# Performance work log

Measured on AMD Instinct MI355X. Metric: run time of the kernel, lower is better.

Reference implementation:

```python
import jax, jax.numpy as jnp
import numpy as np

N, E, D, K, NCONV = 50000, 800000, 64, 3, 6


def setup_inputs() -> dict:
    key = jax.random.key(0)
    ks = jax.random.split(key, 6)
    X = jax.random.normal(ks[0], (N, D), jnp.float32)
    edge_index = jax.random.randint(ks[1], (2, E), 0, N, dtype=jnp.int64)
    edge_weight = jax.random.uniform(ks[2], (E,), jnp.float32)
    H = jax.random.normal(ks[3], (N, D), jnp.float32)
    lambda_max = jnp.ones((1,), jnp.float32) * 2.0  # typical sym-normalized Laplacian bound
    conv_w = jax.random.normal(ks[4], (NCONV, K, D, D), jnp.float32) / np.sqrt(D)
    conv_b = jnp.zeros((NCONV, D), jnp.float32)
    return {"X": X, "edge_index": edge_index, "edge_weight": edge_weight,
            "H": H, "lambda_max": lambda_max, "conv_w": conv_w, "conv_b": conv_b}


def reference(X, edge_index, edge_weight, H, lambda_max, conv_w, conv_b):
    src, dst = edge_index[0], edge_index[1]
    # symmetric normalization: norm_e = w_e / sqrt(deg_src * deg_dst)
    deg = jax.ops.segment_sum(edge_weight, src, num_segments=N)
    dinv = jnp.where(deg > 0, deg ** -0.5, 0.0)
    norm = edge_weight * dinv[src] * dinv[dst]  # [E]
    lam = lambda_max.reshape(())
    c = 2.0 / lam

    def a_prop(v):  # A_norm @ v via scatter-add over edges, [N,D]
        return jax.ops.segment_sum(norm[:, None] * v[src], dst, num_segments=N)

    def l_hat(v):  # (2/lam)(I - A_norm) v - v
        return (c - 1.0) * v - c * a_prop(v)

    def cheb(v, w, b):  # ChebConv order K: sum_k T_k(L_hat) v @ W_k + b
        tx0, tx1 = v, l_hat(v)
        out = tx0 @ w[0] + tx1 @ w[1]
        for k in range(2, K):
            tx2 = 2.0 * l_hat(tx1) - tx0
            out = out + tx2 @ w[k]
            tx0, tx1 = tx1, tx2
        return out + b

    Z = jax.nn.sigmoid(cheb(X, conv_w[0], conv_b[0]) + cheb(H, conv_w[1], conv_b[1]))
    R = jax.nn.sigmoid(cheb(X, conv_w[2], conv_b[2]) + cheb(H, conv_w[3], conv_b[3]))
    H_tilde = jnp.tanh(cheb(X, conv_w[4], conv_b[4]) + cheb(H * R, conv_w[5], conv_b[5]))
    return Z * H_tilde + (1.0 - Z) * H
```

## Files before the change

kernel.cpp:

```cpp
#include <hip/hip_runtime.h>
#include <cstdint>
#include <cstddef>

typedef unsigned int u32;
typedef unsigned short u16;
typedef unsigned long long u64;

#define D 64
#define NCH 512
#define CAP 5120

typedef __attribute__((ext_vector_type(8))) short bf16x8;
typedef __attribute__((ext_vector_type(4))) float f32x4;

static __device__ __forceinline__ float sigmoidf_(float x) {
    return 1.f / (1.f + __expf(-x));
}
static __device__ __forceinline__ u16 f2bf(float x) {
    u32 u = __float_as_uint(x);
    return (u16)((u + 0x7fffu + ((u >> 16) & 1u)) >> 16);
}
static __device__ __forceinline__ u32 packbf2(float a, float b) {
    return (u32)f2bf(a) | ((u32)f2bf(b) << 16);
}
static __device__ __forceinline__ float bflo(u32 u) { return __uint_as_float(u << 16); }
static __device__ __forceinline__ float bfhi(u32 u) { return __uint_as_float(u & 0xffff0000u); }


__global__ void init_kernel(u32* cur_d, u32* cur_s) {
    int t = threadIdx.x;
    cur_d[t] = (u32)(t * CAP);
    cur_s[t] = (u32)(t * CAP);
}

__global__ __launch_bounds__(256) void coarse_kernel(
    const int* __restrict__ src, const int* __restrict__ dst, const float* __restrict__ w,
    u32* cur_d, u32* cur_s,
    u64* __restrict__ slab_d, u32* __restrict__ slab_s,
    int E, int CE) {
    __shared__ u32 hd[256], hs[256], cd[256], cs[256];
    int t = threadIdx.x, c = blockIdx.x;
    hd[t] = 0; hs[t] = 0;
    __syncthreads();
    int e0 = c * CE, e1 = min(E, e0 + CE);
    for (int e = e0 + t; e < e1; e += 256) {
        atomicAdd(&hd[(u32)dst[e] >> 8], 1u);
        atomicAdd(&hs[(u32)src[e] >> 8], 1u);
    }
    __syncthreads();
    cd[t] = atomicAdd(&cur_d[t], hd[t]);
    cs[t] = atomicAdd(&cur_s[t], hs[t]);
    __syncthreads();
    for (int e = e0 + t; e < e1; e += 256) {
        int s = src[e], d = dst[e];
        u32 wb = (u32)f2bf(w[e]);
        u32 pd = atomicAdd(&cd[(u32)d >> 8], 1u);
        u32 ps = atomicAdd(&cs[(u32)s >> 8], 1u);
        if (pd < (u32)(((d >> 8) + 1) * CAP))
            slab_d[pd] = (u64)((u32)s | (((u32)d & 255u) << 16)) | ((u64)wb << 32);
        if (ps < (u32)(((s >> 8) + 1) * CAP))
            slab_s[ps] = ((u32)s & 255u) | (wb << 16);
    }
}

__global__ void bprefix_kernel(const u32* __restrict__ cur_d, u32* __restrict__ bstart, int NB) {
    __shared__ int sd[256];
    int t = threadIdx.x;
    int v = (t < NB) ? min((int)cur_d[t] - t * CAP, CAP) : 0;
    sd[t] = v;
    __syncthreads();
    for (int o = 1; o < 256; o <<= 1) {
        int a = (t >= o) ? sd[t - o] : 0;
        __syncthreads();
        sd[t] += a;
        __syncthreads();
    }
    bstart[t] = (u32)(sd[t] - v);
}

__global__ __launch_bounds__(256) void fine_dst_kernel(
    const u64* __restrict__ slab, const u32* __restrict__ cur_d,
    const u32* __restrict__ bstart, u32* __restrict__ edge4,
    int* __restrict__ cnt, int* __restrict__ row_start, int N_) {
    __shared__ int h[256], sd[256], cur[256];
    int b = blockIdx.x, t = threadIdx.x;
    int m = min((int)cur_d[b] - b * CAP, CAP);
    const u64* rp = slab + (size_t)b * CAP;
    h[t] = 0;
    __syncthreads();
    for (int i = t; i < m; i += 256) atomicAdd(&h[(int)((rp[i] >> 16) & 255u)], 1);
    __syncthreads();
    int v = h[t];
    sd[t] = v;
    __syncthreads();
    for (int o = 1; o < 256; o <<= 1) {
        int a = (t >= o) ? sd[t - o] : 0;
        __syncthreads();
        sd[t] += a;
        __syncthreads();
    }
    int excl = sd[t] - v;
    cur[t] = excl;
    int bs = (int)bstart[b];
    int node = (b << 8) + t;
    if (node < N_) { cnt[node] = v; row_start[node] = bs + excl; }
    __syncthreads();
    for (int i = t; i < m; i += 256) {
        u64 r = rp[i];
        int f = (int)((r >> 16) & 255u);
        int p = atomicAdd(&cur[f], 1);
        edge4[bs + p] = (u32)(r & 0xffffu) | ((u32)(r >> 32) << 16);
    }
}

__global__ __launch_bounds__(256) void fine_deg_kernel(
    const u32* __restrict__ slab_s, const u32* __restrict__ cur_s,
    float* __restrict__ dinv, int N_) {
    __shared__ float dg[256];
    int b = blockIdx.x, t = threadIdx.x;
    int m = min((int)cur_s[b] - b * CAP, CAP);
    const u32* rp = slab_s + (size_t)b * CAP;
    dg[t] = 0.f;
    __syncthreads();
    for (int i = t; i < m; i += 256) {
        u32 r = rp[i];
        atomicAdd(&dg[r & 255u], __uint_as_float(r & 0xffff0000u));
    }
    __syncthreads();
    int node = (b << 8) + t;
    if (node < N_) dinv[node] = (dg[t] > 0.f) ? rsqrtf(dg[t]) : 0.f;
}


__global__ void xh2_kernel(const float* __restrict__ X, const float* __restrict__ H,
                           const float* __restrict__ dinv,
                           u32* __restrict__ XH_u, u32* __restrict__ XH_t, int total) {
    int i = blockIdx.x * blockDim.x + threadIdx.x;
    if (i >= total) return;
    int nn = i >> 6, l = i & 63;
    const float* sp = (l < 32 ? X : H) + (size_t)nn * 64 + ((2 * l) & 63);
    float2 v = *(const float2*)sp;
    float dv = dinv[nn];
    XH_t[i] = packbf2(v.x, v.y);
    XH_u[i] = packbf2(v.x * dv, v.y * dv);
}

__global__ __launch_bounds__(256) void wt_kernel(const float* __restrict__ w, u32* __restrict__ WT) {
    __shared__ float s[64][68];
    int g = blockIdx.x, t = threadIdx.x;
    const float* wp = w + (size_t)g * 4096;
    for (int i = t; i < 1024; i += 256) {
        int k = i >> 4, c4 = (i & 15) * 4;
        *(float4*)&s[k][c4] = *(const float4*)&wp[k * 64 + c4];
    }
    __syncthreads();
    for (int i = t; i < 2048; i += 256) {
        int uk = i & 31, n = i >> 5;
        WT[(size_t)g * 2048 + n * 32 + uk] = packbf2(s[2 * uk][n], s[2 * uk + 1][n]);
    }
}


__global__ __launch_bounds__(256) void lhat128_kernel(
    const u32* __restrict__ vu, const u32* __restrict__ vt, const u32* __restrict__ w0t,
    u32* __restrict__ out_t, u32* __restrict__ out_u,
    const int* __restrict__ rs, const int* __restrict__ cnt, const float* __restrict__ dinv,
    const u32* __restrict__ edges, const float* __restrict__ lam_ptr, int n) {
    int node = (blockIdx.x * blockDim.x + threadIdx.x) >> 6;
    if (node >= n) return;
    int l = threadIdx.x & 63;
    int g = l >> 4, f = l & 15;
    int e0 = rs[node], end = e0 + cnt[node];
    float acc[8];
#pragma unroll
    for (int j = 0; j < 8; j++) acc[j] = 0.f;

    int base = e0;
    for (; base + 16 <= end; base += 16) {
        u32 r0 = edges[base + g];
        u32 r1 = edges[base + 4 + g];
        u32 r2 = edges[base + 8 + g];
        u32 r3 = edges[base + 12 + g];
        const uint4 q0 = *(const uint4*)(vu + (size_t)(r0 & 0xffffu) * 64 + 4 * f);
        const uint4 q1 = *(const uint4*)(vu + (size_t)(r1 & 0xffffu) * 64 + 4 * f);
        const uint4 q2 = *(const uint4*)(vu + (size_t)(r2 & 0xffffu) * 64 + 4 * f);
        const uint4 q3 = *(const uint4*)(vu + (size_t)(r3 & 0xffffu) * 64 + 4 * f);
        float n0 = __uint_as_float(r0 & 0xffff0000u);
        float n1 = __uint_as_float(r1 & 0xffff0000u);
        float n2 = __uint_as_float(r2 & 0xffff0000u);
        float n3 = __uint_as_float(r3 & 0xffff0000u);
        acc[0] += n0 * bflo(q0.x); acc[1] += n0 * bfhi(q0.x);
        acc[2] += n0 * bflo(q0.y); acc[3] += n0 * bfhi(q0.y);
        acc[4] += n0 * bflo(q0.z); acc[5] += n0 * bfhi(q0.z);
        acc[6] += n0 * bflo(q0.w); acc[7] += n0 * bfhi(q0.w);
        acc[0] += n1 * bflo(q1.x); acc[1] += n1 * bfhi(q1.x);
        acc[2] += n1 * bflo(q1.y); acc[3] += n1 * bfhi(q1.y);
        acc[4] += n1 * bflo(q1.z); acc[5] += n1 * bfhi(q1.z);
        acc[6] += n1 * bflo(q1.w); acc[7] += n1 * bfhi(q1.w);
        acc[0] += n2 * bflo(q2.x); acc[1] += n2 * bfhi(q2.x);
        acc[2] += n2 * bflo(q2.y); acc[3] += n2 * bfhi(q2.y);
        acc[4] += n2 * bflo(q2.z); acc[5] += n2 * bfhi(q2.z);
        acc[6] += n2 * bflo(q2.w); acc[7] += n2 * bfhi(q2.w);
        acc[0] += n3 * bflo(q3.x); acc[1] += n3 * bfhi(q3.x);
        acc[2] += n3 * bflo(q3.y); acc[3] += n3 * bfhi(q3.y);
        acc[4] += n3 * bflo(q3.z); acc[5] += n3 * bfhi(q3.z);
        acc[6] += n3 * bflo(q3.w); acc[7] += n3 * bfhi(q3.w);
    }
    for (; base < end; base += 4) {
        int ei = base + g;
        u32 r0 = (ei < end) ? edges[ei] : 0u;
        const uint4 q0 = *(const uint4*)(vu + (size_t)(r0 & 0xffffu) * 64 + 4 * f);
        float n0 = __uint_as_float(r0 & 0xffff0000u);
        acc[0] += n0 * bflo(q0.x); acc[1] += n0 * bfhi(q0.x);
        acc[2] += n0 * bflo(q0.y); acc[3] += n0 * bfhi(q0.y);
        acc[4] += n0 * bflo(q0.z); acc[5] += n0 * bfhi(q0.z);
        acc[6] += n0 * bflo(q0.w); acc[7] += n0 * bfhi(q0.w);
    }
#pragma unroll
    for (int m = 16; m <= 32; m <<= 1)
#pragma unroll
        for (int j = 0; j < 8; j++) acc[j] += __shfl_xor(acc[j], m);

    const uint4 sv = *(const uint4*)(vt + (size_t)node * 64 + 4 * f);
    float self[8];
    self[0] = bflo(sv.x); self[1] = bfhi(sv.x);
    self[2] = bflo(sv.y); self[3] = bfhi(sv.y);
    self[4] = bflo(sv.z); self[5] = bfhi(sv.z);
    self[6] = bflo(sv.w); self[7] = bfhi(sv.w);
    float c = 2.f / lam_ptr[0];
    float dv = dinv[node];
    float rx[8];
#pragma unroll
    for (int j = 0; j < 8; j++) rx[j] = (c - 1.f) * self[j] - (c * dv) * acc[j];
    if (w0t) {
        const uint4 wv4 = *(const uint4*)(w0t + (size_t)node * 64 + 4 * f);
        rx[0] = 2.f * rx[0] - bflo(wv4.x); rx[1] = 2.f * rx[1] - bfhi(wv4.x);
        rx[2] = 2.f * rx[2] - bflo(wv4.y); rx[3] = 2.f * rx[3] - bfhi(wv4.y);
        rx[4] = 2.f * rx[4] - bflo(wv4.z); rx[5] = 2.f * rx[5] - bfhi(wv4.z);
        rx[6] = 2.f * rx[6] - bflo(wv4.w); rx[7] = 2.f * rx[7] - bfhi(wv4.w);
    }
    if (l < 16) {
        uint4 o;
        o.x = packbf2(rx[0], rx[1]); o.y = packbf2(rx[2], rx[3]);
        o.z = packbf2(rx[4], rx[5]); o.w = packbf2(rx[6], rx[7]);
        *(uint4*)(out_t + (size_t)node * 64 + 4 * f) = o;
        if (out_u) {
            uint4 ou;
            ou.x = packbf2(rx[0] * dv, rx[1] * dv); ou.y = packbf2(rx[2] * dv, rx[3] * dv);
            ou.z = packbf2(rx[4] * dv, rx[5] * dv); ou.w = packbf2(rx[6] * dv, rx[7] * dv);
            *(uint4*)(out_u + (size_t)node * 64 + 4 * f) = ou;
        }
    }
}

__global__ __launch_bounds__(256) void lhat64_kernel(
    const u32* __restrict__ vu, const u32* __restrict__ vt, const u32* __restrict__ w0t,
    u32* __restrict__ out_t, u32* __restrict__ out_u,
    const int* __restrict__ rs, const int* __restrict__ cnt, const float* __restrict__ dinv,
    const u32* __restrict__ edges, const float* __restrict__ lam_ptr, int n) {
    int node = (blockIdx.x * blockDim.x + threadIdx.x) >> 6;
    if (node >= n) return;
    int l = threadIdx.x & 63;
    int g = l >> 3, f = l & 7;
    int e0 = rs[node], end = e0 + cnt[node];
    float acc[8];
#pragma unroll
    for (int j = 0; j < 8; j++) acc[j] = 0.f;

    int base = e0;
    for (; base + 16 <= end; base += 16) {
        u32 r0 = edges[base + g];
        u32 r1 = edges[base + 8 + g];
        const uint4 q0 = *(const uint4*)(vu + (size_t)(r0 & 0xffffu) * 32 + 4 * f);
        const uint4 q1 = *(const uint4*)(vu + (size_t)(r1 & 0xffffu) * 32 + 4 * f);
        float n0 = __uint_as_float(r0 & 0xffff0000u);
        float n1 = __uint_as_float(r1 & 0xffff0000u);
        acc[0] += n0 * bflo(q0.x); acc[1] += n0 * bfhi(q0.x);
        acc[2] += n0 * bflo(q0.y); acc[3] += n0 * bfhi(q0.y);
        acc[4] += n0 * bflo(q0.z); acc[5] += n0 * bfhi(q0.z);
        acc[6] += n0 * bflo(q0.w); acc[7] += n0 * bfhi(q0.w);
        acc[0] += n1 * bflo(q1.x); acc[1] += n1 * bfhi(q1.x);
        acc[2] += n1 * bflo(q1.y); acc[3] += n1 * bfhi(q1.y);
        acc[4] += n1 * bflo(q1.z); acc[5] += n1 * bfhi(q1.z);
        acc[6] += n1 * bflo(q1.w); acc[7] += n1 * bfhi(q1.w);
    }
    for (; base < end; base += 8) {
        int ei = base + g;
        u32 r0 = (ei < end) ? edges[ei] : 0u;
        const uint4 q0 = *(const uint4*)(vu + (size_t)(r0 & 0xffffu) * 32 + 4 * f);
        float n0 = __uint_as_float(r0 & 0xffff0000u);
        acc[0] += n0 * bflo(q0.x); acc[1] += n0 * bfhi(q0.x);
        acc[2] += n0 * bflo(q0.y); acc[3] += n0 * bfhi(q0.y);
        acc[4] += n0 * bflo(q0.z); acc[5] += n0 * bfhi(q0.z);
        acc[6] += n0 * bflo(q0.w); acc[7] += n0 * bfhi(q0.w);
    }
#pragma unroll
    for (int m = 8; m <= 32; m <<= 1)
#pragma unroll
        for (int j = 0; j < 8; j++) acc[j] += __shfl_xor(acc[j], m);

    const uint4 sv = *(const uint4*)(vt + (size_t)node * 32 + 4 * f);
    float self[8];
    self[0] = bflo(sv.x); self[1] = bfhi(sv.x);
    self[2] = bflo(sv.y); self[3] = bfhi(sv.y);
    self[4] = bflo(sv.z); self[5] = bfhi(sv.z);
    self[6] = bflo(sv.w); self[7] = bfhi(sv.w);
    float c = 2.f / lam_ptr[0];
    float dv = dinv[node];
    float rx[8];
#pragma unroll
    for (int j = 0; j < 8; j++) rx[j] = (c - 1.f) * self[j] - (c * dv) * acc[j];
    if (w0t) {
        const uint4 wv4 = *(const uint4*)(w0t + (size_t)node * 32 + 4 * f);
        rx[0] = 2.f * rx[0] - bflo(wv4.x); rx[1] = 2.f * rx[1] - bfhi(wv4.x);
        rx[2] = 2.f * rx[2] - bflo(wv4.y); rx[3] = 2.f * rx[3] - bfhi(wv4.y);
        rx[4] = 2.f * rx[4] - bflo(wv4.z); rx[5] = 2.f * rx[5] - bfhi(wv4.z);
        rx[6] = 2.f * rx[6] - bflo(wv4.w); rx[7] = 2.f * rx[7] - bfhi(wv4.w);
    }
    if (l < 8) {
        uint4 o;
        o.x = packbf2(rx[0], rx[1]); o.y = packbf2(rx[2], rx[3]);
        o.z = packbf2(rx[4], rx[5]); o.w = packbf2(rx[6], rx[7]);
        *(uint4*)(out_t + (size_t)node * 32 + 4 * f) = o;
        if (out_u) {
            uint4 ou;
            ou.x = packbf2(rx[0] * dv, rx[1] * dv); ou.y = packbf2(rx[2] * dv, rx[3] * dv);
            ou.z = packbf2(rx[4] * dv, rx[5] * dv); ou.w = packbf2(rx[6] * dv, rx[7] * dv);
            *(uint4*)(out_u + (size_t)node * 32 + 4 * f) = ou;
        }
    }
}

__global__ __launch_bounds__(256) void gemm_gate_kernel(
    const u32* __restrict__ A0, const u32* __restrict__ A1, const u32* __restrict__ A2,
    const u32* __restrict__ WT, const float* __restrict__ convb,
    const float* __restrict__ Hf, const float* __restrict__ dinv,
    float* __restrict__ Zb, float* __restrict__ Sh,
    u16* __restrict__ HR_t, u16* __restrict__ HR_u, int n) {
    __shared__ u32 As[128][68];
    int t = threadIdx.x;
    int wv = t >> 6, l = t & 63;
    int q = l >> 4, ml = l & 15;
    int r0 = blockIdx.x * 128;

    f32x4 S[3][2][4];
#pragma unroll
    for (int tg = 0; tg < 3; tg++)
#pragma unroll
        for (int mi = 0; mi < 2; mi++)
#pragma unroll
            for (int ni = 0; ni < 4; ni++) S[tg][mi][ni] = (f32x4){0.f, 0.f, 0.f, 0.f};

    for (int kt = 0; kt < 3; kt++) {
        const u32* Ap = (kt == 0) ? A0 : ((kt == 1) ? A1 : A2);
        int ar = t >> 1, ac = (t & 1) * 32;
        int gr = r0 + ar; if (gr >= n) gr = n - 1;
        const u32* gp = Ap + (size_t)gr * 64 + ac;
        uint4 v0 = *(const uint4*)(gp +  0);
        uint4 v1 = *(const uint4*)(gp +  4);
        uint4 v2 = *(const uint4*)(gp +  8);
        uint4 v3 = *(const uint4*)(gp + 12);
        uint4 v4 = *(const uint4*)(gp + 16);
        uint4 v5 = *(const uint4*)(gp + 20);
        uint4 v6 = *(const uint4*)(gp + 24);
        uint4 v7 = *(const uint4*)(gp + 28);
        __syncthreads();
        *(uint4*)&As[ar][ac +  0] = v0;
        *(uint4*)&As[ar][ac +  4] = v1;
        *(uint4*)&As[ar][ac +  8] = v2;
        *(uint4*)&As[ar][ac + 12] = v3;
        *(uint4*)&As[ar][ac + 16] = v4;
        *(uint4*)&As[ar][ac + 20] = v5;
        *(uint4*)&As[ar][ac + 24] = v6;
        *(uint4*)&As[ar][ac + 28] = v7;
        __syncthreads();

        bf16x8 af[2][2][2];
#pragma unroll
        for (int mi = 0; mi < 2; mi++)
#pragma unroll
            for (int h = 0; h < 2; h++)
#pragma unroll
                for (int hf = 0; hf < 2; hf++)
                    af[mi][h][hf] = *(const bf16x8*)&As[wv * 32 + mi * 16 + ml][hf * 32 + h * 16 + q * 4];

#pragma unroll
        for (int cg = 0; cg < 5; cg++) {
            int hf = cg & 1, tg = cg >> 1;
            const u32* Wp = WT + (size_t)(cg * 3 + kt) * 2048 + ml * 32 + q * 4;
#pragma unroll
            for (int h = 0; h < 2; h++) {
                bf16x8 bw[4];
#pragma unroll
                for (int ni = 0; ni < 4; ni++)
                    bw[ni] = *(const bf16x8*)(Wp + ni * 512 + h * 16);
#pragma unroll
                for (int mi = 0; mi < 2; mi++)
#pragma unroll
                    for (int ni = 0; ni < 4; ni++)
                        S[tg][mi][ni] = __builtin_amdgcn_mfma_f32_16x16x32_bf16(
                            af[mi][h][hf], bw[ni], S[tg][mi][ni], 0, 0, 0);
            }
        }
    }
#pragma unroll
    for (int ni = 0; ni < 4; ni++) {
        int col = ni * 16 + ml;
        float bz = convb[col] + convb[64 + col];
        float br = convb[128 + col] + convb[192 + col];
#pragma unroll
        for (int mi = 0; mi < 2; mi++)
#pragma unroll
            for (int reg = 0; reg < 4; reg++) {
                int row = r0 + wv * 32 + mi * 16 + q * 4 + reg;
                if (row < n) {
                    size_t o = (size_t)row * 64 + col;
                    float z = sigmoidf_(S[0][mi][ni][reg] + bz);
                    float r = sigmoidf_(S[1][mi][ni][reg] + br);
                    float hr = Hf[o] * r;
                    float dv = dinv[row];
                    Zb[o] = z;
                    Sh[o] = S[2][mi][ni][reg];
                    HR_t[o] = f2bf(hr);
                    HR_u[o] = f2bf(hr * dv);
                }
            }
    }
}

__global__ __launch_bounds__(256) void gemm_final_kernel(
    const u32* __restrict__ A0, const u32* __restrict__ A1, const u32* __restrict__ A2,
    const u32* __restrict__ WT, const float* __restrict__ convb,
    const float* __restrict__ Zb, const float* __restrict__ Sh, const float* __restrict__ Hf,
    float* __restrict__ outp, int n) {
    __shared__ u32 As[128][36];
    int t = threadIdx.x;
    int wv = t >> 6, l = t & 63;
    int q = l >> 4, ml = l & 15;
    int r0 = blockIdx.x * 128;

    f32x4 S[2][4];
#pragma unroll
    for (int mi = 0; mi < 2; mi++)
#pragma unroll
        for (int ni = 0; ni < 4; ni++) S[mi][ni] = (f32x4){0.f, 0.f, 0.f, 0.f};

    for (int kt = 0; kt < 3; kt++) {
        const u32* Ap = (kt == 0) ? A0 : ((kt == 1) ? A1 : A2);
        int ar = t >> 1, ac = (t & 1) * 16;
        int gr = r0 + ar; if (gr >= n) gr = n - 1;
        const u32* gp = Ap + (size_t)gr * 32 + ac;
        uint4 v0 = *(const uint4*)(gp +  0);
        uint4 v1 = *(const uint4*)(gp +  4);
        uint4 v2 = *(const uint4*)(gp +  8);
        uint4 v3 = *(const uint4*)(gp + 12);
        __syncthreads();
        *(uint4*)&As[ar][ac +  0] = v0;
        *(uint4*)&As[ar][ac +  4] = v1;
        *(uint4*)&As[ar][ac +  8] = v2;
        *(uint4*)&As[ar][ac + 12] = v3;
        __syncthreads();

        const u32* Wp = WT + (size_t)(15 + kt) * 2048 + ml * 32 + q * 4;
#pragma unroll
        for (int h = 0; h < 2; h++) {
            bf16x8 bw[4];
#pragma unroll
            for (int ni = 0; ni < 4; ni++)
                bw[ni] = *(const bf16x8*)(Wp + ni * 512 + h * 16);
#pragma unroll
            for (int mi = 0; mi < 2; mi++) {
                bf16x8 afr = *(const bf16x8*)&As[wv * 32 + mi * 16 + ml][h * 16 + q * 4];
#pragma unroll
                for (int ni = 0; ni < 4; ni++)
                    S[mi][ni] = __builtin_amdgcn_mfma_f32_16x16x32_bf16(afr, bw[ni], S[mi][ni], 0, 0, 0);
            }
        }
    }
#pragma unroll
    for (int ni = 0; ni < 4; ni++) {
        int col = ni * 16 + ml;
        float bh = convb[256 + col] + convb[320 + col];
#pragma unroll
        for (int mi = 0; mi < 2; mi++)
#pragma unroll
            for (int reg = 0; reg < 4; reg++) {
                int row = r0 + wv * 32 + mi * 16 + q * 4 + reg;
                if (row < n) {
                    size_t o = (size_t)row * 64 + col;
                    float z = Zb[o];
                    float ht = tanhf(S[mi][ni][reg] + Sh[o] + bh);
                    outp[o] = z * ht + (1.f - z) * Hf[o];
                }
            }
    }
}


extern "C" void kernel_launch(void* const* d_in, const int* in_sizes, int n_in,
                              void* d_out, int out_size, void* d_ws, size_t ws_size,
                              hipStream_t stream) {
    const float* X     = (const float*)d_in[0];
    const int*   ei    = (const int*)d_in[1];
    const float* ew    = (const float*)d_in[2];
    const float* H     = (const float*)d_in[3];
    const float* lam   = (const float*)d_in[4];
    const float* convw = (const float*)d_in[5];
    const float* convb = (const float*)d_in[6];
    float* out = (float*)d_out;

    const int N = in_sizes[0] / D;
    const int E = in_sizes[2];
    const int* src = ei;
    const int* dst = ei + E;

    const int NB = (N + 255) >> 8;
    const int CE = (E + NCH - 1) / NCH;

    char* p = (char*)d_ws;
    auto alloc = [&](size_t bytes) {
        void* r = (void*)p;
        p += (bytes + 255) & ~(size_t)255;
        return r;
    };
    float* Zb   = (float*)alloc((size_t)N * 64 * 4);
    float* Sh   = (float*)alloc((size_t)N * 64 * 4);
    u32* XH_u = (u32*)alloc((size_t)N * 64 * 4);
    u32* XH_t = (u32*)alloc((size_t)N * 64 * 4);
    u32* T1_u = (u32*)alloc((size_t)N * 64 * 4);
    u32* T1_t = (u32*)alloc((size_t)N * 64 * 4);
    u32* T2_t = (u32*)alloc((size_t)N * 64 * 4);
    u16* HR_u = (u16*)alloc((size_t)N * 64 * 2);
    u16* HR_t = (u16*)alloc((size_t)N * 64 * 2);
    u16* U1_u = (u16*)alloc((size_t)N * 64 * 2);
    u16* U1_t = (u16*)alloc((size_t)N * 64 * 2);
    u16* U2_t = (u16*)alloc((size_t)N * 64 * 2);
    u32* edge4 = (u32*)alloc((size_t)E * 4);
    u64* slab_d = (u64*)alloc((size_t)NB * CAP * 8);
    u32* slab_s = (u32*)alloc((size_t)NB * CAP * 4);
    u32* cur_d  = (u32*)alloc(256 * 4);
    u32* cur_s  = (u32*)alloc(256 * 4);
    u32* bstart = (u32*)alloc(256 * 4);
    int* cnt       = (int*)alloc((size_t)N * 4);
    int* row_start = (int*)alloc((size_t)N * 4);
    float* dinv    = (float*)alloc((size_t)N * 4);
    u32* WT = (u32*)alloc((size_t)18 * 2048 * 4);

    const int BLK = 256;
    const int gND  = (N * D + BLK - 1) / BLK;
    const int gWav = gND;
    const int gx   = (N + 127) / 128;

    init_kernel<<<1, 256, 0, stream>>>(cur_d, cur_s);
    coarse_kernel<<<NCH, BLK, 0, stream>>>(src, dst, ew, cur_d, cur_s, slab_d, slab_s, E, CE);
    bprefix_kernel<<<1, 256, 0, stream>>>(cur_d, bstart, NB);
    fine_dst_kernel<<<NB, BLK, 0, stream>>>(slab_d, cur_d, bstart, edge4, cnt, row_start, N);
    fine_deg_kernel<<<NB, BLK, 0, stream>>>(slab_s, cur_s, dinv, N);

    wt_kernel<<<18, BLK, 0, stream>>>(convw, WT);
    xh2_kernel<<<gND, BLK, 0, stream>>>(X, H, dinv, XH_u, XH_t, N * D);

    lhat128_kernel<<<gWav, BLK, 0, stream>>>(XH_u, XH_t, nullptr, T1_t, T1_u,
                                             row_start, cnt, dinv, edge4, lam, N);
    lhat128_kernel<<<gWav, BLK, 0, stream>>>(T1_u, T1_t, XH_t, T2_t, nullptr,
                                             row_start, cnt, dinv, edge4, lam, N);

    gemm_gate_kernel<<<gx, BLK, 0, stream>>>(XH_t, T1_t, T2_t, WT, convb, H, dinv,
                                             Zb, Sh, HR_t, HR_u, N);

    lhat64_kernel<<<gWav, BLK, 0, stream>>>((const u32*)HR_u, (const u32*)HR_t, nullptr,
                                            (u32*)U1_t, (u32*)U1_u,
                                            row_start, cnt, dinv, edge4, lam, N);
    lhat64_kernel<<<gWav, BLK, 0, stream>>>((const u32*)U1_u, (const u32*)U1_t, (const u32*)HR_t,
                                            (u32*)U2_t, nullptr,
                                            row_start, cnt, dinv, edge4, lam, N);

    gemm_final_kernel<<<gx, BLK, 0, stream>>>((const u32*)HR_t, (const u32*)U1_t, (const u32*)U2_t,
                                              WT, convb, Zb, Sh, H, out, N);
}
```

Baseline: 339.3 us.

## Load GEMM A fragments directly from global memory, dropping LDS staging

Both GEMM kernels now have each wavefront own 16 rows and read its bf16 A-fragments straight from global memory into registers, instead of staging a 128-row tile through shared memory with two barriers per k-step. Blocks shrink to 64 rows, so the grid doubles and fewer accumulators are held per wave. This removes LDS traffic and syncs and may raise occupancy, but the direct loads are less coalesced and the weight fragments are reloaded from memory per 16 rows rather than per 32.

```diff
diff --git a/kernel.cpp b/kernel.cpp
--- a/kernel.cpp
+++ b/kernel.cpp
@@ -337,53 +337,26 @@
     const float* __restrict__ Hf, const float* __restrict__ dinv,
     float* __restrict__ Zb, float* __restrict__ Sh,
     u16* __restrict__ HR_t, u16* __restrict__ HR_u, int n) {
-    __shared__ u32 As[128][68];
     int t = threadIdx.x;
     int wv = t >> 6, l = t & 63;
     int q = l >> 4, ml = l & 15;
-    int r0 = blockIdx.x * 128;
-
-    f32x4 S[3][2][4];
+    int R = blockIdx.x * 64 + wv * 16;
+    int ar = R + ml; if (ar >= n) ar = n - 1;
+
+    f32x4 S[3][4];
 #pragma unroll
     for (int tg = 0; tg < 3; tg++)
 #pragma unroll
-        for (int mi = 0; mi < 2; mi++)
-#pragma unroll
-            for (int ni = 0; ni < 4; ni++) S[tg][mi][ni] = (f32x4){0.f, 0.f, 0.f, 0.f};
+        for (int ni = 0; ni < 4; ni++) S[tg][ni] = (f32x4){0.f, 0.f, 0.f, 0.f};
 
     for (int kt = 0; kt < 3; kt++) {
         const u32* Ap = (kt == 0) ? A0 : ((kt == 1) ? A1 : A2);
-        int ar = t >> 1, ac = (t & 1) * 32;
-        int gr = r0 + ar; if (gr >= n) gr = n - 1;
-        const u32* gp = Ap + (size_t)gr * 64 + ac;
-        uint4 v0 = *(const uint4*)(gp +  0);
-        uint4 v1 = *(const uint4*)(gp +  4);
-        uint4 v2 = *(const uint4*)(gp +  8);
-        uint4 v3 = *(const uint4*)(gp + 12);
-        uint4 v4 = *(const uint4*)(gp + 16);
-        uint4 v5 = *(const uint4*)(gp + 20);
-        uint4 v6 = *(const uint4*)(gp + 24);
-        uint4 v7 = *(const uint4*)(gp + 28);
-        __syncthreads();
-        *(uint4*)&As[ar][ac +  0] = v0;
-        *(uint4*)&As[ar][ac +  4] = v1;
-        *(uint4*)&As[ar][ac +  8] = v2;
-        *(uint4*)&As[ar][ac + 12] = v3;
-        *(uint4*)&As[ar][ac + 16] = v4;
-        *(uint4*)&As[ar][ac + 20] = v5;
-        *(uint4*)&As[ar][ac + 24] = v6;
-        *(uint4*)&As[ar][ac + 28] = v7;
-        __syncthreads();
-
-        bf16x8 af[2][2][2];
-#pragma unroll
-        for (int mi = 0; mi < 2; mi++)
-#pragma unroll
-            for (int h = 0; h < 2; h++)
-#pragma unroll
-                for (int hf = 0; hf < 2; hf++)
-                    af[mi][h][hf] = *(const bf16x8*)&As[wv * 32 + mi * 16 + ml][hf * 32 + h * 16 + q * 4];
-
+        const u32* ap = Ap + (size_t)ar * 64 + q * 4;
+        bf16x8 af[2][2];
+        af[0][0] = *(const bf16x8*)(ap +  0);
+        af[1][0] = *(const bf16x8*)(ap + 16);
+        af[0][1] = *(const bf16x8*)(ap + 32);
+        af[1][1] = *(const bf16x8*)(ap + 48);
 #pragma unroll
         for (int cg = 0; cg < 5; cg++) {
             int hf = cg & 1, tg = cg >> 1;
@@ -395,11 +368,9 @@
                 for (int ni = 0; ni < 4; ni++)
                     bw[ni] = *(const bf16x8*)(Wp + ni * 512 + h * 16);
 #pragma unroll
-                for (int mi = 0; mi < 2; mi++)
-#pragma unroll
-                    for (int ni = 0; ni < 4; ni++)
-                        S[tg][mi][ni] = __builtin_amdgcn_mfma_f32_16x16x32_bf16(
-                            af[mi][h][hf], bw[ni], S[tg][mi][ni], 0, 0, 0);
+                for (int ni = 0; ni < 4; ni++)
+                    S[tg][ni] = __builtin_amdgcn_mfma_f32_16x16x32_bf16(
+                        af[h][hf], bw[ni], S[tg][ni], 0, 0, 0);
             }
         }
     }
@@ -409,22 +380,20 @@
         float bz = convb[col] + convb[64 + col];
         float br = convb[128 + col] + convb[192 + col];
 #pragma unroll
-        for (int mi = 0; mi < 2; mi++)
-#pragma unroll
-            for (int reg = 0; reg < 4; reg++) {
-                int row = r0 + wv * 32 + mi * 16 + q * 4 + reg;
-                if (row < n) {
-                    size_t o = (size_t)row * 64 + col;
-                    float z = sigmoidf_(S[0][mi][ni][reg] + bz);
-                    float r = sigmoidf_(S[1][mi][ni][reg] + br);
-                    float hr = Hf[o] * r;
-                    float dv = dinv[row];
-                    Zb[o] = z;
-                    Sh[o] = S[2][mi][ni][reg];
-                    HR_t[o] = f2bf(hr);
-                    HR_u[o] = f2bf(hr * dv);
-                }
+        for (int reg = 0; reg < 4; reg++) {
+            int row = R + q * 4 + reg;
+            if (row < n) {
+                size_t o = (size_t)row * 64 + col;
+                float z = sigmoidf_(S[0][ni][reg] + bz);
+                float r = sigmoidf_(S[1][ni][reg] + br);
+                float hr = Hf[o] * r;
+                float dv = dinv[row];
+                Zb[o] = z;
+                Sh[o] = S[2][ni][reg];
+                HR_t[o] = f2bf(hr);
+                HR_u[o] = f2bf(hr * dv);
             }
+        }
     }
 }
 
@@ -433,34 +402,22 @@
     const u32* __restrict__ WT, const float* __restrict__ convb,
     const float* __restrict__ Zb, const float* __restrict__ Sh, const float* __restrict__ Hf,
     float* __restrict__ outp, int n) {
-    __shared__ u32 As[128][36];
     int t = threadIdx.x;
     int wv = t >> 6, l = t & 63;
     int q = l >> 4, ml = l & 15;
-    int r0 = blockIdx.x * 128;
-
-    f32x4 S[2][4];
-#pragma unroll
-    for (int mi = 0; mi < 2; mi++)
-#pragma unroll
-        for (int ni = 0; ni < 4; ni++) S[mi][ni] = (f32x4){0.f, 0.f, 0.f, 0.f};
+    int R = blockIdx.x * 64 + wv * 16;
+    int ar = R + ml; if (ar >= n) ar = n - 1;
+
+    f32x4 S[4];
+#pragma unroll
+    for (int ni = 0; ni < 4; ni++) S[ni] = (f32x4){0.f, 0.f, 0.f, 0.f};
 
     for (int kt = 0; kt < 3; kt++) {
         const u32* Ap = (kt == 0) ? A0 : ((kt == 1) ? A1 : A2);
-        int ar = t >> 1, ac = (t & 1) * 16;
-        int gr = r0 + ar; if (gr >= n) gr = n - 1;
-        const u32* gp = Ap + (size_t)gr * 32 + ac;
-        uint4 v0 = *(const uint4*)(gp +  0);
-        uint4 v1 = *(const uint4*)(gp +  4);
-        uint4 v2 = *(const uint4*)(gp +  8);
-        uint4 v3 = *(const uint4*)(gp + 12);
-        __syncthreads();
-        *(uint4*)&As[ar][ac +  0] = v0;
-        *(uint4*)&As[ar][ac +  4] = v1;
-        *(uint4*)&As[ar][ac +  8] = v2;
-        *(uint4*)&As[ar][ac + 12] = v3;
-        __syncthreads();
-
+        const u32* ap = Ap + (size_t)ar * 32 + q * 4;
+        bf16x8 af[2];
+        af[0] = *(const bf16x8*)(ap +  0);
+        af[1] = *(const bf16x8*)(ap + 16);
         const u32* Wp = WT + (size_t)(15 + kt) * 2048 + ml * 32 + q * 4;
 #pragma unroll
         for (int h = 0; h < 2; h++) {
@@ -469,12 +426,8 @@
             for (int ni = 0; ni < 4; ni++)
                 bw[ni] = *(const bf16x8*)(Wp + ni * 512 + h * 16);
 #pragma unroll
-            for (int mi = 0; mi < 2; mi++) {
-                bf16x8 afr = *(const bf16x8*)&As[wv * 32 + mi * 16 + ml][h * 16 + q * 4];
-#pragma unroll
-                for (int ni = 0; ni < 4; ni++)
-                    S[mi][ni] = __builtin_amdgcn_mfma_f32_16x16x32_bf16(afr, bw[ni], S[mi][ni], 0, 0, 0);
-            }
+            for (int ni = 0; ni < 4; ni++)
+                S[ni] = __builtin_amdgcn_mfma_f32_16x16x32_bf16(af[h], bw[ni], S[ni], 0, 0, 0);
         }
     }
 #pragma unroll
@@ -482,17 +435,15 @@
         int col = ni * 16 + ml;
         float bh = convb[256 + col] + convb[320 + col];
 #pragma unroll
-        for (int mi = 0; mi < 2; mi++)
-#pragma unroll
-            for (int reg = 0; reg < 4; reg++) {
-                int row = r0 + wv * 32 + mi * 16 + q * 4 + reg;
-                if (row < n) {
-                    size_t o = (size_t)row * 64 + col;
-                    float z = Zb[o];
-                    float ht = tanhf(S[mi][ni][reg] + Sh[o] + bh);
-                    outp[o] = z * ht + (1.f - z) * Hf[o];
-                }
+        for (int reg = 0; reg < 4; reg++) {
+            int row = R + q * 4 + reg;
+            if (row < n) {
+                size_t o = (size_t)row * 64 + col;
+                float z = Zb[o];
+                float ht = tanhf(S[ni][reg] + Sh[o] + bh);
+                outp[o] = z * ht + (1.f - z) * Hf[o];
             }
+        }
     }
 }
 
@@ -549,7 +500,7 @@
     const int BLK = 256;
     const int gND  = (N * D + BLK - 1) / BLK;
     const int gWav = gND;
-    const int gx   = (N + 127) / 128;
+    const int gx64 = (N + 63) / 64;
 
     init_kernel<<<1, 256, 0, stream>>>(cur_d, cur_s);
     coarse_kernel<<<NCH, BLK, 0, stream>>>(src, dst, ew, cur_d, cur_s, slab_d, slab_s, E, CE);
@@ -565,8 +516,8 @@
     lhat128_kernel<<<gWav, BLK, 0, stream>>>(T1_u, T1_t, XH_t, T2_t, nullptr,
                                              row_start, cnt, dinv, edge4, lam, N);
 
-    gemm_gate_kernel<<<gx, BLK, 0, stream>>>(XH_t, T1_t, T2_t, WT, convb, H, dinv,
-                                             Zb, Sh, HR_t, HR_u, N);
+    gemm_gate_kernel<<<gx64, BLK, 0, stream>>>(XH_t, T1_t, T2_t, WT, convb, H, dinv,
+                                               Zb, Sh, HR_t, HR_u, N);
 
     lhat64_kernel<<<gWav, BLK, 0, stream>>>((const u32*)HR_u, (const u32*)HR_t, nullptr,
                                             (u32*)U1_t, (u32*)U1_u,
@@ -575,6 +526,6 @@
                                             (u32*)U2_t, nullptr,
                                             row_start, cnt, dinv, edge4, lam, N);
 
-    gemm_final_kernel<<<gx, BLK, 0, stream>>>((const u32*)HR_t, (const u32*)U1_t, (const u32*)U2_t,
-                                              WT, convb, Zb, Sh, H, out, N);
-}
+    gemm_final_kernel<<<gx64, BLK, 0, stream>>>((const u32*)HR_t, (const u32*)U1_t, (const u32*)U2_t,
+                                                WT, convb, Zb, Sh, H, out, N);
+}
```

Result: slower. 368.3 us (+8.6%).
